# Kernel optimization log

Measured on AMD Instinct MI355X. Metric: run time of the kernel, lower is better.

## Reference

```python
import jax, jax.numpy as jnp
import numpy as np

B, T, C, MULT, ND, H = 32, 512, 384, 4, 16, 1024
D = C * MULT            # input_dim = 1536
SIZE, STRIDE = 4, 2     # stack kernel / stride
L = (T - SIZE) // STRIDE + 1  # 255 stacked frames
MAXF = 512
SCALE = float(H) ** 0.5  # config.scale == None -> sqrt(hidden_size)


def setup_inputs() -> dict:
    key = jax.random.key(0)
    ks = jax.random.split(key, 8)
    return {
        "spikes": jax.random.normal(ks[0], (B, T, C), jnp.float32),
        "spikes_mask": jax.random.randint(ks[1], (B, T), 0, 2).astype(jnp.int32),
        "spikes_timestamp": jax.random.randint(ks[2], (B, T), 0, MAXF),
        "date_idx": jax.random.randint(ks[3], (B,), 0, ND),
        "W_embed": jax.random.normal(ks[4], (ND, D, C), jnp.float32) * 0.02,
        "b_embed": jnp.zeros((ND, D), jnp.float32),
        "W_proj": jax.random.normal(ks[5], (H, SIZE * D), jnp.float32) * 0.02,
        "b_proj": jnp.zeros((H,), jnp.float32),
        "pos_table": jax.random.normal(ks[6], (MAXF, H), jnp.float32) * 0.02,
    }


def reference(spikes, spikes_mask, spikes_timestamp, date_idx,
              W_embed, b_embed, W_proj, b_proj, pos_table):
    # --- adaptive per-date linear: grouped GEMM instead of per-sample loop ---
    Wg = W_embed[date_idx]          # [B, D, C]
    bg = b_embed[date_idx]          # [B, D]
    x = jnp.einsum('btc,bdc->btd', spikes, Wg) + bg[:, None, :]  # [B, T, D]
    # act * scale (torch 'gelu' is exact erf gelu)
    x = jax.nn.gelu(x, approximate=False) * SCALE
    # --- unfold-stack: windows of SIZE frames, stride STRIDE ---
    starts = jnp.arange(L) * STRIDE
    win = starts[:, None] + jnp.arange(SIZE)          # [L, SIZE]
    patches = x[:, win, :].reshape(B, L, SIZE * D)    # [B, L, SIZE*D] (kh-major = torch unfold order)
    x = patches @ W_proj.T + b_proj                   # [B, L, H]
    # stacked mask: product of window mask entries
    mask = jnp.prod(spikes_mask[:, win], axis=-1).astype(spikes_mask.dtype)  # [B, L]
    ts = spikes_timestamp[:, :L]                      # [B, L]
    # positional embedding add; dropout p=0 -> identity
    x = x + pos_table[ts]
    return x, mask, ts
```

## Files before the change

### kernel.cpp

```cpp
#include <hip/hip_runtime.h>
#include <hip/hip_bf16.h>

#define B_    32
#define T_    512
#define C_    384
#define D_    1536
#define H_    1024
#define L_    255
#define KP_   6144
#define ND_   16

#define BUFB 49152
#define G2BUF 32768

using f32x4 = __attribute__((ext_vector_type(4))) float;
using s16x8 = __attribute__((ext_vector_type(8))) short;
using i32x4 = __attribute__((ext_vector_type(4))) int;
using i32x8 = __attribute__((ext_vector_type(8))) int;

__device__ __forceinline__ void gld_lds16(const void* g, void* l) {
    __builtin_amdgcn_global_load_lds(
        (const __attribute__((address_space(1))) void*)g,
        (__attribute__((address_space(3))) void*)l,
        16, 0, 0);
}

__device__ __forceinline__ f32x4 MFMA(s16x8 a, s16x8 b, f32x4 c) {
    return __builtin_amdgcn_mfma_f32_16x16x32_bf16(a, b, c, 0, 0, 0);
}

__device__ __forceinline__ f32x4 MFMA8(i32x8 a, i32x8 b, f32x4 c) {
    return __builtin_amdgcn_mfma_scale_f32_16x16x128_f8f6f4(
        a, b, c, 0, 0, 0, 0x7F7F7F7F, 0, 0x7B7B7B7B);
}

__global__ __launch_bounds__(256) void prep(
    const float* __restrict__ sp, const float* __restrict__ we,
    const float* __restrict__ wp, const int* __restrict__ mIn,
    const int* __restrict__ tIn,
    __hip_bfloat16* __restrict__ spB, __hip_bfloat16* __restrict__ weB,
    unsigned char* __restrict__ wp8, float* __restrict__ out) {
    int id = blockIdx.x * 256 + threadIdx.x;
    if (id < 3932160) {
        const float* src; __hip_bfloat16* dst; int idx;
        if (id < 1572864) { src = sp; dst = spB; idx = id; }
        else              { src = we; dst = weB; idx = id - 1572864; }
        float4 v = reinterpret_cast<const float4*>(src)[idx];
        __hip_bfloat16 o[4] = {__float2bfloat16(v.x), __float2bfloat16(v.y),
                               __float2bfloat16(v.z), __float2bfloat16(v.w)};
        reinterpret_cast<ushort4*>(dst)[idx] = *reinterpret_cast<ushort4*>(o);
    } else if (id < 5505024) {
        int idx = id - 3932160;
        float4 v = reinterpret_cast<const float4*>(wp)[idx];
        int w = __builtin_amdgcn_cvt_pk_fp8_f32(v.x * 16.f, v.y * 16.f, 0, false);
        w = __builtin_amdgcn_cvt_pk_fp8_f32(v.z * 16.f, v.w * 16.f, w, true);
        reinterpret_cast<int*>(wp8)[idx] = w;
    } else {
        int i = id - 5505024;
        if (i < B_ * L_) {
            int b = i / L_, l = i % L_;
            const int* mb = mIn + b * T_ + 2 * l;
            int m = mb[0] * mb[1] * mb[2] * mb[3];
            const size_t offM = (size_t)B_ * L_ * H_;
            out[offM + i] = (float)m;
            out[offM + (size_t)B_ * L_ + i] = (float)tIn[b * T_ + l];
        }
    }
}

__device__ __forceinline__ void tile_compute(const char* la, const char* lb,
                                             f32x4 (&acc)[4][4],
                                             int rA, int rB, int g) {
    const int sxA = rA & 7, sxB = rB & 7;
    s16x8 af0[4], bf0[4], af1[4], bf1[4];
    #pragma unroll
    for (int mi = 0; mi < 4; ++mi)
        af0[mi] = *(const s16x8*)(la + rA * 128 + mi * 2048 + ((g ^ sxA) << 4));
    #pragma unroll
    for (int ni = 0; ni < 4; ++ni)
        bf0[ni] = *(const s16x8*)(lb + rB * 128 + ni * 2048 + ((g ^ sxB) << 4));
    #pragma unroll
    for (int mi = 0; mi < 4; ++mi)
        af1[mi] = *(const s16x8*)(la + rA * 128 + mi * 2048 + (((4 + g) ^ sxA) << 4));
    #pragma unroll
    for (int ni = 0; ni < 4; ++ni)
        bf1[ni] = *(const s16x8*)(lb + rB * 128 + ni * 2048 + (((4 + g) ^ sxB) << 4));
    asm volatile("s_waitcnt lgkmcnt(8)" ::: "memory");
    __builtin_amdgcn_sched_barrier(0);
    __builtin_amdgcn_s_setprio(1);
    #pragma unroll
    for (int mi = 0; mi < 4; ++mi)
        #pragma unroll
        for (int ni = 0; ni < 4; ++ni)
            acc[mi][ni] = MFMA(af0[mi], bf0[ni], acc[mi][ni]);
    __builtin_amdgcn_s_setprio(0);
    asm volatile("s_waitcnt lgkmcnt(0)" ::: "memory");
    __builtin_amdgcn_sched_barrier(0);
    __builtin_amdgcn_s_setprio(1);
    #pragma unroll
    for (int mi = 0; mi < 4; ++mi)
        #pragma unroll
        for (int ni = 0; ni < 4; ++ni)
            acc[mi][ni] = MFMA(af1[mi], bf1[ni], acc[mi][ni]);
    __builtin_amdgcn_s_setprio(0);
}

__global__ __launch_bounds__(512, 2) void gemm1_embed(
    const __hip_bfloat16* __restrict__ Sp,
    const __hip_bfloat16* __restrict__ We,
    const float* __restrict__ bEmb,
    const int* __restrict__ dateIdx,
    unsigned char* __restrict__ X18) {
    extern __shared__ __align__(16) char lds[];
    const int tid  = threadIdx.x;
    const int lane = tid & 63, wid = tid >> 6;
    const int wr = wid >> 1, wc = wid & 1;
    const int id   = blockIdx.x;
    const int xcd  = id & 7, slot = id >> 3;
    const int b    = xcd * 4 + slot / 24;
    const int tile = slot % 24;
    const int m0   = (tile % 2) * 256;
    const int n0   = (tile / 2) * 128;
    const int didx = dateIdx[b];
    const __hip_bfloat16* A  = Sp + (size_t)b * T_ * C_;
    const __hip_bfloat16* Bm = We + (size_t)didx * D_ * C_;
    const int KT = C_ / 64;

    auto stage = [&](int kt, int buf) {
        char* lA = lds + buf * BUFB;
        char* lB = lA + 32768;
        int k0 = kt * 64;
        #pragma unroll
        for (int i = 0; i < 4; ++i) {
            int p = i * 512 + tid;
            int row = p >> 3;
            int clog = (p & 7) ^ (row & 7);
            gld_lds16(A + (size_t)(m0 + row) * C_ + k0 + clog * 8,
                      lA + (i * 512 + wid * 64) * 16);
        }
        #pragma unroll
        for (int i = 0; i < 2; ++i) {
            int p = i * 512 + tid;
            int row = p >> 3;
            int clog = (p & 7) ^ (row & 7);
            gld_lds16(Bm + (size_t)(n0 + row) * C_ + k0 + clog * 8,
                      lB + (i * 512 + wid * 64) * 16);
        }
    };

    f32x4 acc[4][4] = {};
    const int rl = lane & 15, g = lane >> 4;
    const int rA = wr * 64 + rl, rB = wc * 64 + rl;

    stage(0, 0);
    stage(1, 1);
    for (int kt = 0; kt < KT - 2; ++kt) {
        stage(kt + 2, (kt + 2) % 3);
        asm volatile("s_waitcnt vmcnt(12)" ::: "memory");
        __builtin_amdgcn_s_barrier();
        const char* la = lds + (kt % 3) * BUFB;
        tile_compute(la, la + 32768, acc, rA, rB, g);
        __builtin_amdgcn_s_barrier();
    }
    asm volatile("s_waitcnt vmcnt(6)" ::: "memory");
    __builtin_amdgcn_s_barrier();
    {
        const char* la = lds + ((KT - 2) % 3) * BUFB;
        tile_compute(la, la + 32768, acc, rA, rB, g);
    }
    asm volatile("s_waitcnt vmcnt(0)" ::: "memory");
    __builtin_amdgcn_s_barrier();
    {
        const char* la = lds + ((KT - 1) % 3) * BUFB;
        tile_compute(la, la + 32768, acc, rA, rB, g);
    }

    #pragma unroll
    for (int mi = 0; mi < 4; ++mi) {
        #pragma unroll
        for (int ni = 0; ni < 4; ++ni) {
            int col = n0 + wc * 64 + ni * 16 + rl;
            float bg = bEmb[didx * D_ + col];
            #pragma unroll
            for (int r = 0; r < 4; ++r) {
                int row = m0 + wr * 64 + mi * 16 + g * 4 + r;
                float v = acc[mi][ni][r] + bg;
                float gl = 0.5f * v * (1.0f + erff(v * 0.70710678118f)) * 32.0f;
                int pk = __builtin_amdgcn_cvt_pk_fp8_f32(gl, gl, 0, false);
                X18[((size_t)b * T_ + row) * D_ + col] = (unsigned char)pk;
            }
        }
    }
}

__global__ __launch_bounds__(256, 2) void gemm2_proj(
    const unsigned char* __restrict__ X18,
    const unsigned char* __restrict__ Wp8,
    const float* __restrict__ bProj,
    const float* __restrict__ posTab,
    const int* __restrict__ tsIn,
    float* __restrict__ outX) {
    extern __shared__ __align__(16) char lds[];
    const int tid  = threadIdx.x;
    const int lane = tid & 63, wid = tid >> 6;
    const int wm = wid >> 1, wn = wid & 1;
    const int id   = blockIdx.x;
    const int xcd  = id & 7, slot = id >> 3;
    const int b    = xcd * 4 + (slot >> 4);
    const int t    = slot & 15;
    const int m0   = (t & 1) * 128;
    const int n0   = (t >> 1) * 128;
    const unsigned char* Xb = X18 + (size_t)b * T_ * D_;
    const int KT = 48;

    const unsigned char* aP[4]; const unsigned char* bP[4]; int dstC[4];
    #pragma unroll
    for (int i = 0; i < 4; ++i) {
        int p = i * 256 + tid;
        int row = p >> 3;
        int c = (p & 7) ^ (row & 7);
        int l = m0 + row; if (l > 254) l = 254;
        aP[i] = Xb + (size_t)(2 * l) * D_ + c * 16;
        bP[i] = Wp8 + (size_t)(n0 + row) * KP_ + c * 16;
        dstC[i] = (i * 256 + wid * 64) * 16;
    }
    auto stage = [&](int kt, char* buf) {
        int ko = (kt & 3) * D_ + (kt >> 2) * 128;
        #pragma unroll
        for (int i = 0; i < 4; ++i) {
            gld_lds16(aP[i] + ko, buf + dstC[i]);
            gld_lds16(bP[i] + ko, buf + 16384 + dstC[i]);
        }
    };

    const int rl = lane & 15, g = lane >> 4, sx = rl & 7;
    const int ck0 = ((2 * g) ^ sx) << 4;
    const int ck1 = ((2 * g + 1) ^ sx) << 4;
    int aOff[4], bOff[4];
    #pragma unroll
    for (int mi = 0; mi < 4; ++mi) aOff[mi] = (wm * 64 + mi * 16 + rl) * 128;
    #pragma unroll
    for (int ni = 0; ni < 4; ++ni) bOff[ni] = 16384 + (wn * 64 + ni * 16 + rl) * 128;

    union u8x32 { i32x8 v; i32x4 h[2]; };
    f32x4 acc[4][4] = {};

    stage(0, lds);
    for (int u = 0; u < KT; ++u) {
        char* cur = lds + (u & 1) * G2BUF;
        if (u + 1 < KT) stage(u + 1, lds + ((u + 1) & 1) * G2BUF);
        if (u + 1 < KT) { asm volatile("s_waitcnt vmcnt(8)" ::: "memory"); }
        else            { asm volatile("s_waitcnt vmcnt(0)" ::: "memory"); }
        __builtin_amdgcn_s_barrier();

        u8x32 A[4], Bv[4];
        #pragma unroll
        for (int mi = 0; mi < 4; ++mi) {
            A[mi].h[0] = *(const i32x4*)(cur + aOff[mi] + ck0);
            A[mi].h[1] = *(const i32x4*)(cur + aOff[mi] + ck1);
        }
        #pragma unroll
        for (int ni = 0; ni < 4; ++ni) {
            Bv[ni].h[0] = *(const i32x4*)(cur + bOff[ni] + ck0);
            Bv[ni].h[1] = *(const i32x4*)(cur + bOff[ni] + ck1);
        }
        #pragma unroll
        for (int ni = 0; ni < 4; ++ni)
            #pragma unroll
            for (int mi = 0; mi < 4; ++mi)
                acc[mi][ni] = MFMA8(A[mi].v, Bv[ni].v, acc[mi][ni]);
        __builtin_amdgcn_s_barrier();
    }

    #pragma unroll
    for (int mi = 0; mi < 4; ++mi) {
        #pragma unroll
        for (int ni = 0; ni < 4; ++ni) {
            int h = n0 + wn * 64 + ni * 16 + rl;
            float bp = bProj[h];
            #pragma unroll
            for (int r = 0; r < 4; ++r) {
                int l = m0 + wm * 64 + mi * 16 + g * 4 + r;
                if (l < L_) {
                    int tsv = tsIn[b * T_ + l];
                    float v = acc[mi][ni][r] + bp + posTab[(size_t)tsv * H_ + h];
                    outX[((size_t)b * L_ + l) * H_ + h] = v;
                }
            }
        }
    }
}

extern "C" void kernel_launch(void* const* d_in, const int* in_sizes, int n_in,
                              void* d_out, int out_size, void* d_ws, size_t ws_size,
                              hipStream_t stream) {
    (void)in_sizes; (void)n_in; (void)out_size; (void)ws_size;
    const float* spikes  = (const float*)d_in[0];
    const int*   smask   = (const int*)d_in[1];
    const int*   sts     = (const int*)d_in[2];
    const int*   dateIdx = (const int*)d_in[3];
    const float* Wemb    = (const float*)d_in[4];
    const float* bEmb    = (const float*)d_in[5];
    const float* Wproj   = (const float*)d_in[6];
    const float* bProj   = (const float*)d_in[7];
    const float* posTab  = (const float*)d_in[8];
    float* out = (float*)d_out;

    char* ws = (char*)d_ws;
    unsigned char*  X18 = (unsigned char*)(ws);
    __hip_bfloat16* SpB = (__hip_bfloat16*)(ws + 25165824);
    __hip_bfloat16* WeB = (__hip_bfloat16*)(ws + 37748736);
    unsigned char*  Wp8 = (unsigned char*)(ws + 56623104);

    hipFuncSetAttribute((const void*)gemm1_embed,
                        hipFuncAttributeMaxDynamicSharedMemorySize, 3 * BUFB);
    hipFuncSetAttribute((const void*)gemm2_proj,
                        hipFuncAttributeMaxDynamicSharedMemorySize, 2 * G2BUF);

    prep<<<21536, 256, 0, stream>>>(spikes, Wemb, Wproj, smask, sts,
                                    SpB, WeB, Wp8, out);

    gemm1_embed<<<768, 512, 3 * BUFB, stream>>>(SpB, WeB, bEmb, dateIdx, X18);

    gemm2_proj<<<512, 256, 2 * G2BUF, stream>>>(X18, Wp8, bProj, posTab, sts, out);
}
```

Baseline: 133.6 us.

## Load gemm2 A operand directly from global into registers, keep only B in LDS

```diff
diff --git a/kernel.cpp b/kernel.cpp
--- a/kernel.cpp
+++ b/kernel.cpp
@@ -11,7 +11,6 @@
 #define ND_   16
 
 #define BUFB 49152
-#define G2BUF 32768
 
 using f32x4 = __attribute__((ext_vector_type(4))) float;
 using s16x8 = __attribute__((ext_vector_type(8))) short;
@@ -200,7 +199,7 @@
     const float* __restrict__ posTab,
     const int* __restrict__ tsIn,
     float* __restrict__ outX) {
-    extern __shared__ __align__(16) char lds[];
+    __shared__ __align__(16) char ldsB[2][16384];
     const int tid  = threadIdx.x;
     const int lane = tid & 63, wid = tid >> 6;
     const int wm = wid >> 1, wn = wid & 1;
@@ -213,63 +212,78 @@
     const unsigned char* Xb = X18 + (size_t)b * T_ * D_;
     const int KT = 48;
 
-    const unsigned char* aP[4]; const unsigned char* bP[4]; int dstC[4];
+    const unsigned char* bP[4]; int dstC[4];
     #pragma unroll
     for (int i = 0; i < 4; ++i) {
         int p = i * 256 + tid;
         int row = p >> 3;
         int c = (p & 7) ^ (row & 7);
-        int l = m0 + row; if (l > 254) l = 254;
-        aP[i] = Xb + (size_t)(2 * l) * D_ + c * 16;
         bP[i] = Wp8 + (size_t)(n0 + row) * KP_ + c * 16;
         dstC[i] = (i * 256 + wid * 64) * 16;
     }
-    auto stage = [&](int kt, char* buf) {
-        int ko = (kt & 3) * D_ + (kt >> 2) * 128;
-        #pragma unroll
-        for (int i = 0; i < 4; ++i) {
-            gld_lds16(aP[i] + ko, buf + dstC[i]);
-            gld_lds16(bP[i] + ko, buf + 16384 + dstC[i]);
-        }
+    auto kofs = [&](int kt) { return (kt & 3) * D_ + (kt >> 2) * 128; };
+    auto stageB = [&](int kt, int buf) {
+        int ko = kofs(kt);
+        #pragma unroll
+        for (int i = 0; i < 4; ++i)
+            gld_lds16(bP[i] + ko, &ldsB[buf][dstC[i]]);
     };
 
     const int rl = lane & 15, g = lane >> 4, sx = rl & 7;
+    const unsigned char* aAddr[4];
+    #pragma unroll
+    for (int mi = 0; mi < 4; ++mi) {
+        int l = m0 + wm * 64 + mi * 16 + rl; if (l > 254) l = 254;
+        aAddr[mi] = Xb + (size_t)(2 * l) * D_ + g * 32;
+    }
+    auto loadA = [&](i32x8 (&dst)[4], int kt) {
+        int ko = kofs(kt);
+        #pragma unroll
+        for (int mi = 0; mi < 4; ++mi) {
+            i32x4 lo = *(const i32x4*)(aAddr[mi] + ko);
+            i32x4 hi = *(const i32x4*)(aAddr[mi] + ko + 16);
+            dst[mi] = __builtin_shufflevector(lo, hi, 0, 1, 2, 3, 4, 5, 6, 7);
+        }
+    };
+
     const int ck0 = ((2 * g) ^ sx) << 4;
     const int ck1 = ((2 * g + 1) ^ sx) << 4;
-    int aOff[4], bOff[4];
-    #pragma unroll
-    for (int mi = 0; mi < 4; ++mi) aOff[mi] = (wm * 64 + mi * 16 + rl) * 128;
-    #pragma unroll
-    for (int ni = 0; ni < 4; ++ni) bOff[ni] = 16384 + (wn * 64 + ni * 16 + rl) * 128;
+    int bOff[4];
+    #pragma unroll
+    for (int ni = 0; ni < 4; ++ni) bOff[ni] = (wn * 64 + ni * 16 + rl) * 128;
 
     union u8x32 { i32x8 v; i32x4 h[2]; };
     f32x4 acc[4][4] = {};
-
-    stage(0, lds);
+    i32x8 Acur[4], Anxt[4];
+
+    stageB(0, 0);
+    loadA(Acur, 0);
     for (int u = 0; u < KT; ++u) {
-        char* cur = lds + (u & 1) * G2BUF;
-        if (u + 1 < KT) stage(u + 1, lds + ((u + 1) & 1) * G2BUF);
-        if (u + 1 < KT) { asm volatile("s_waitcnt vmcnt(8)" ::: "memory"); }
-        else            { asm volatile("s_waitcnt vmcnt(0)" ::: "memory"); }
+        int buf = u & 1;
+        if (u + 1 < KT) {
+            stageB(u + 1, buf ^ 1);
+            loadA(Anxt, u + 1);
+            asm volatile("s_waitcnt vmcnt(12)" ::: "memory");
+        } else {
+            asm volatile("s_waitcnt vmcnt(0)" ::: "memory");
+        }
         __builtin_amdgcn_s_barrier();
 
-        u8x32 A[4], Bv[4];
-        #pragma unroll
-        for (int mi = 0; mi < 4; ++mi) {
-            A[mi].h[0] = *(const i32x4*)(cur + aOff[mi] + ck0);
-            A[mi].h[1] = *(const i32x4*)(cur + aOff[mi] + ck1);
-        }
+        u8x32 Bv[4];
         #pragma unroll
         for (int ni = 0; ni < 4; ++ni) {
-            Bv[ni].h[0] = *(const i32x4*)(cur + bOff[ni] + ck0);
-            Bv[ni].h[1] = *(const i32x4*)(cur + bOff[ni] + ck1);
+            Bv[ni].h[0] = *(const i32x4*)(&ldsB[buf][0] + bOff[ni] + ck0);
+            Bv[ni].h[1] = *(const i32x4*)(&ldsB[buf][0] + bOff[ni] + ck1);
         }
         #pragma unroll
         for (int ni = 0; ni < 4; ++ni)
             #pragma unroll
             for (int mi = 0; mi < 4; ++mi)
-                acc[mi][ni] = MFMA8(A[mi].v, Bv[ni].v, acc[mi][ni]);
+                acc[mi][ni] = MFMA8(Acur[mi], Bv[ni].v, acc[mi][ni]);
         __builtin_amdgcn_s_barrier();
+
+        #pragma unroll
+        for (int mi = 0; mi < 4; ++mi) Acur[mi] = Anxt[mi];
     }
 
     #pragma unroll
@@ -314,13 +328,11 @@
 
     hipFuncSetAttribute((const void*)gemm1_embed,
                         hipFuncAttributeMaxDynamicSharedMemorySize, 3 * BUFB);
-    hipFuncSetAttribute((const void*)gemm2_proj,
-                        hipFuncAttributeMaxDynamicSharedMemorySize, 2 * G2BUF);
 
     prep<<<21536, 256, 0, stream>>>(spikes, Wemb, Wproj, smask, sts,
                                     SpB, WeB, Wp8, out);
 
     gemm1_embed<<<768, 512, 3 * BUFB, stream>>>(SpB, WeB, bEmb, dateIdx, X18);
 
-    gemm2_proj<<<512, 256, 2 * G2BUF, stream>>>(X18, Wp8, bProj, posTab, sts, out);
-}
+    gemm2_proj<<<512, 256, 0, stream>>>(X18, Wp8, bProj, posTab, sts, out);
+}
```

New measurement: 195.9 us. +46.6%, slower.
